# Performance work log

Measured on AMD Instinct MI355X. Metric: run time of the kernel, lower is better.

The kernel has to match this reference:

```python
import jax, jax.numpy as jnp
import numpy as np

DIM = 256
NUM_HEADS = 8
HEAD_DIM = DIM // NUM_HEADS


def rope_sincos(H, W, head_dim, dtype=jnp.float32):
    n = head_dim // 4
    angle = 1.0 / (10000.0 ** jnp.linspace(0.0, 1.0, n))
    angle = jnp.repeat(angle, 2)  # (head_dim//2,)
    ph = jnp.arange(H, dtype=dtype)[:, None] * angle[None, :]  # (H, d/2)
    pw = jnp.arange(W, dtype=dtype)[:, None] * angle[None, :]  # (W, d/2)
    sin_h = jnp.broadcast_to(jnp.sin(ph)[:, None, :], (H, W, 2 * n))
    sin_w = jnp.broadcast_to(jnp.sin(pw)[None, :, :], (H, W, 2 * n))
    cos_h = jnp.broadcast_to(jnp.cos(ph)[:, None, :], (H, W, 2 * n))
    cos_w = jnp.broadcast_to(jnp.cos(pw)[None, :, :], (H, W, 2 * n))
    sin = jnp.concatenate([sin_h, sin_w], -1).reshape(H * W, head_dim)
    cos = jnp.concatenate([cos_h, cos_w], -1).reshape(H * W, head_dim)
    return sin, cos


def rotate_every_two(x):
    x1 = x[..., 0::2]
    x2 = x[..., 1::2]
    return jnp.stack([-x2, x1], axis=-1).reshape(x.shape)


def theta_shift(x, sin, cos):
    return x * cos + rotate_every_two(x) * sin


def conv1x1(x, w, b):
    # x: (B,C,H,W), w: (O,C,1,1)
    return jnp.einsum('bchw,oc->bohw', x, w[:, :, 0, 0]) + b[None, :, None, None]


def depthwise5x5(x, w, b):
    # x: (B,C,H,W), w: (C,1,5,5), groups=C
    y = jax.lax.conv_general_dilated(
        x, w, window_strides=(1, 1), padding=((2, 2), (2, 2)),
        feature_group_count=x.shape[1],
        dimension_numbers=('NCHW', 'OIHW', 'NCHW'))
    return y + b[None, :, None, None]


def setup_inputs() -> dict:
    key = jax.random.key(0)
    ks = jax.random.split(key, 7)
    B, C, H, W = 8, DIM, 64, 64
    x = jax.random.normal(ks[0], (B, C, H, W), dtype=jnp.float32)
    qkvo_w = 0.02 * jax.random.normal(ks[1], (4 * C, C, 1, 1), dtype=jnp.float32)
    qkvo_b = jnp.zeros((4 * C,), dtype=jnp.float32)
    lepe_w = 0.02 * jax.random.normal(ks[2], (C, 1, 5, 5), dtype=jnp.float32)
    lepe_b = jnp.zeros((C,), dtype=jnp.float32)
    proj_w = 0.02 * jax.random.normal(ks[3], (C, C, 1, 1), dtype=jnp.float32)
    proj_b = jnp.zeros((C,), dtype=jnp.float32)
    return {'x': x, 'qkvo_w': qkvo_w, 'qkvo_b': qkvo_b,
            'lepe_w': lepe_w, 'lepe_b': lepe_b,
            'proj_w': proj_w, 'proj_b': proj_b}


def reference(x, qkvo_w, qkvo_b, lepe_w, lepe_b, proj_w, proj_b):
    B, C, H, W = x.shape
    n, d = NUM_HEADS, HEAD_DIM
    L = H * W
    scale = d ** (-0.5)

    sin, cos = rope_sincos(H, W, d, dtype=x.dtype)  # (L, d)

    qkvo = conv1x1(x, qkvo_w, qkvo_b)          # (B, 4C, H, W)
    qkv = qkvo[:, :3 * C]                       # (B, 3C, H, W)
    o = qkvo[:, 3 * C:]                         # (B, C, H, W)
    lepe = depthwise5x5(qkv[:, 2 * C:], lepe_w, lepe_b)  # (B, C, H, W)

    # 'b (m n d) h w -> m b n (h w) d'
    qkv_r = qkv.reshape(B, 3, n, d, H * W).transpose(1, 0, 2, 4, 3)  # (3,B,n,L,d)
    q, k, v = qkv_r[0], qkv_r[1], qkv_r[2]

    q = jax.nn.elu(q) + 1.0
    k = jax.nn.elu(k) + 1.0

    kmean = k.mean(axis=2, keepdims=True)               # (B,n,1,d)
    z = jnp.einsum('bnld,bnmd->bnlm', q, kmean) * scale  # (B,n,L,1)

    q = theta_shift(q, sin, cos)
    k = theta_shift(k, sin, cos)

    c = (scale / L) ** 0.5
    kv = jnp.einsum('bnld,bnle->bnde', k * c, v * c)     # (B,n,d,d)
    vmean = v.mean(axis=2, keepdims=True)                # (B,n,1,d)

    res = jnp.einsum('bnld,bnde->bnle', q, kv) * (1.0 + 1.0 / (z + 1e-6)) - z * vmean
    # 'b n (h w) d -> b (n d) h w'
    res = res.reshape(B, n, H, W, d).transpose(0, 1, 4, 2, 3).reshape(B, C, H, W)
    res = res + lepe
    return conv1x1(res * o, proj_w, proj_b)
```

## Files before the change

### kernel.cpp

```cpp
#include <hip/hip_runtime.h>
#include <math.h>

typedef unsigned short u16;
typedef unsigned int u32;
typedef unsigned long long u64;
typedef __attribute__((ext_vector_type(8))) short short8;
typedef __attribute__((ext_vector_type(4))) float f32x4;
typedef __attribute__((ext_vector_type(16))) float f32x16;

static constexpr float SCALE = 0.17677669529663687f;
static constexpr float C2    = 0.17677669529663687f / 4096.f;

__device__ __forceinline__ float bf2f(u16 u){
  union { u32 i; float f; } v; v.i = ((u32)u) << 16; return v.f;
}
__device__ __forceinline__ u16 f2bf(float f){
  union { float fl; u32 i; } v; v.fl = f;
  u32 r = v.i + 0x7fffu + ((v.i >> 16) & 1u);
  return (u16)(r >> 16);
}
__device__ __forceinline__ float eluP(float x){ return x > 0.f ? x + 1.f : __expf(x); }
__device__ __forceinline__ float rfreq(int j){
  const float t[8] = {1.f, 0.2682695795f, 0.0719685673f, 0.0193069773f,
                      0.0051794747f, 0.0013894955f, 0.0003727594f, 1e-4f};
  return t[j];
}
__device__ __forceinline__ void gload16(const u16* g, u16* l){
  __builtin_amdgcn_global_load_lds(
      (const __attribute__((address_space(1))) u32*)g,
      (__attribute__((address_space(3))) u32*)l, 16, 0, 0);
}

__global__ __launch_bounds__(256) void k_pre(
    const float* __restrict__ x, const float* __restrict__ qw, const float* __restrict__ pw,
    u16* __restrict__ XT, u16* __restrict__ Whi, u16* __restrict__ Wlo,
    u16* __restrict__ Phi, u16* __restrict__ Plo, float* __restrict__ KM0)
{
  if (blockIdx.z < 8){
    __shared__ float t[64][65];
    int l0 = blockIdx.x * 64, c0 = blockIdx.y * 64, b = blockIdx.z;
    const float* xp = x + (((long)b * 256 + c0) << 12) + l0;
    #pragma unroll
    for (int rep = 0; rep < 4; rep++){
      int idx = threadIdx.x + rep * 256;
      int r = idx >> 4, ch = (idx & 15) * 4;
      float4 f = *(const float4*)&xp[((long)r << 12) + ch];
      t[r][ch] = f.x; t[r][ch+1] = f.y; t[r][ch+2] = f.z; t[r][ch+3] = f.w;
    }
    __syncthreads();
    int r2 = threadIdx.x >> 2, c8 = (threadIdx.x & 3) * 16;
    u32 w[8];
    #pragma unroll
    for (int j = 0; j < 8; j++){
      float v0 = t[c8 + 2*j][r2], v1 = t[c8 + 2*j + 1][r2];
      w[j] = (u32)f2bf(v0) | ((u32)f2bf(v1) << 16);
    }
    long ob = (((long)b << 12) << 8) + ((long)(l0 + r2) << 8) + c0 + c8;
    *(uint4*)&XT[ob]     = make_uint4(w[0], w[1], w[2], w[3]);
    *(uint4*)&XT[ob + 8] = make_uint4(w[4], w[5], w[6], w[7]);
  } else {
    int bid = (blockIdx.z - 8) * 256 + blockIdx.y * 64 + blockIdx.x;
    int idx = bid * 256 + threadIdx.x;
    if (idx < 262144){
      float v = qw[idx]; u16 h = f2bf(v);
      Whi[idx] = h; Wlo[idx] = f2bf(v - bf2f(h));
    }
    if (idx < 65536){
      float v = pw[idx]; u16 h = f2bf(v);
      Phi[idx] = h; Plo[idx] = f2bf(v - bf2f(h));
    }
    if (bid == 0){
      #pragma unroll
      for (int i = 0; i < 16; i++) KM0[threadIdx.x + i * 256] = 0.f;
    }
  }
}

__global__ __launch_bounds__(256) void k_gemmA(
    const u16* __restrict__ Whi_, const u16* __restrict__ Wlo_,
    const u16* __restrict__ Bh_,
    const float* __restrict__ bias,
    u16* __restrict__ Q16, u16* __restrict__ K16,
    u16* __restrict__ V16, u16* __restrict__ O16,
    float* __restrict__ KMb, float* __restrict__ VMb)
{
  __shared__ __align__(16) u16 AhS[4096];
  __shared__ __align__(16) u16 AlS[4096];
  __shared__ __align__(16) u16 BhS[4096];
  __shared__ float scs[2][8][64];
  const int tid = threadIdx.x;
  const int nt = blockIdx.x, mt = blockIdx.y, b = blockIdx.z;
  const int m0 = mt * 128, n0 = nt * 128;
  const int wave = tid >> 6, lane = tid & 63;
  const int wm = wave & 1, wn = wave >> 1, qu = lane >> 4, ln = lane & 15;

  #pragma unroll
  for (int r = 0; r < 2; r++){
    int idx = tid + r * 256;
    int jj = idx >> 6, pp = idx & 63;
    float sn, cs; sincosf(rfreq(jj) * (float)pp, &sn, &cs);
    scs[0][jj][pp] = sn; scs[1][jj][pp] = cs;
  }

  const u16* bhp = Bh_ + (((long)b << 12) << 8);

  const int l4 = lane >> 2, c4 = lane & 3;
  const int gch = (c4 ^ (l4 & 3)) * 8;
  const int fch = (qu ^ (ln & 3)) * 8;

  f32x4 acc[4][4];
  #pragma unroll
  for (int im = 0; im < 4; im++)
    #pragma unroll
    for (int in = 0; in < 4; in++)
      #pragma unroll
      for (int r = 0; r < 4; r++) acc[im][in][r] = 0.f;

  for (int kk = 0; kk < 256; kk += 32){
    #pragma unroll
    for (int t = 0; t < 2; t++){
      int rw = wave * 32 + t * 16;
      int ga = (m0 + rw + l4) * 256 + kk + gch;
      long gb = (long)(n0 + rw + l4) * 256 + kk + gch;
      gload16(&Whi_[ga], &AhS[rw * 32]);
      gload16(&Wlo_[ga], &AlS[rw * 32]);
      gload16(&bhp[gb],  &BhS[rw * 32]);
    }
    __syncthreads();
    short8 fbh[4];
    #pragma unroll
    for (int in = 0; in < 4; in++){
      int row = wn * 64 + in * 16 + ln;
      fbh[in] = *(short8*)&BhS[row * 32 + fch];
    }
    #pragma unroll
    for (int im = 0; im < 4; im++){
      int row = wm * 64 + im * 16 + ln;
      short8 fah = *(short8*)&AhS[row * 32 + fch];
      short8 fal = *(short8*)&AlS[row * 32 + fch];
      #pragma unroll
      for (int in = 0; in < 4; in++){
        acc[im][in] = __builtin_amdgcn_mfma_f32_16x16x32_bf16(fah, fbh[in], acc[im][in], 0, 0, 0);
        acc[im][in] = __builtin_amdgcn_mfma_f32_16x16x32_bf16(fal, fbh[in], acc[im][in], 0, 0, 0);
      }
    }
    __syncthreads();
  }

  const int range = m0 >> 8;
  u16* dst = (range == 0) ? Q16 : (range == 1) ? K16 : (range == 2) ? V16 : O16;
  #pragma unroll
  for (int im = 0; im < 4; im++){
    const int mb = m0 + wm * 64 + im * 16 + qu * 4;
    float v[4][4];
    #pragma unroll
    for (int r = 0; r < 4; r++){
      float bia = bias[mb + r];
      #pragma unroll
      for (int in = 0; in < 4; in++){
        float t = acc[im][in][r] + bia;
        v[r][in] = (range < 2) ? eluP(t) : t;
      }
    }
    if (range == 1 || range == 2){
      float* mbuf = (range == 1) ? KMb : VMb;
      #pragma unroll
      for (int r = 0; r < 4; r++){
        float s = v[r][0] + v[r][1] + v[r][2] + v[r][3];
        s += __shfl_xor(s, 1); s += __shfl_xor(s, 2);
        s += __shfl_xor(s, 4); s += __shfl_xor(s, 8);
        if (ln == 0) atomicAdd(&mbuf[b * 256 + ((mb + r) & 255)], s);
      }
    }
    if (range == 1){
      const int p0 = (mb & 31) >> 1;
      #pragma unroll
      for (int half = 0; half < 2; half++){
        int p = p0 + half, j = p & 7;
        #pragma unroll
        for (int in = 0; in < 4; in++){
          int n = n0 + wn * 64 + in * 16 + ln;
          int pos = (p < 8) ? (n >> 6) : (n & 63);
          float sn = scs[0][j][pos], cs = scs[1][j][pos];
          float a = v[2*half][in], bb = v[2*half+1][in];
          v[2*half][in]   = a * cs - bb * sn;
          v[2*half+1][in] = bb * cs + a * sn;
        }
      }
    }
    #pragma unroll
    for (int r = 0; r < 4; r++){
      u16* rowp = dst + (((long)b * 256 + ((mb + r) & 255)) << 12);
      #pragma unroll
      for (int in = 0; in < 4; in++){
        int n = n0 + wn * 64 + in * 16 + ln;
        rowp[n] = f2bf(v[r][in]);
      }
    }
  }
}

__global__ __launch_bounds__(256) void k_mid(
    const u16* __restrict__ K16, const u16* __restrict__ V16,
    const float* __restrict__ lw, const float* __restrict__ lb,
    u16* __restrict__ Tb16, float* __restrict__ KVb)
{
  if (blockIdx.y < 256){
    __shared__ float tile[20][68];
    __shared__ float wl[25];
    int ht = blockIdx.x, ch = blockIdx.y, b = blockIdx.z;
    int h0 = ht * 16;
    const u16* vp = V16 + (((long)b * 256 + ch) << 12);
    if (threadIdx.x < 25) wl[threadIdx.x] = lw[ch * 25 + threadIdx.x];
    for (int idx = threadIdx.x; idx < 20 * 68; idx += 256){
      int r = idx / 68, c = idx % 68;
      int gh = h0 + r - 2, gw = c - 2;
      float v = 0.f;
      if (gh >= 0 && gh < 64 && gw >= 0 && gw < 64) v = bf2f(vp[(gh << 6) + gw]);
      tile[r][c] = v;
    }
    __syncthreads();
    const float bia = lb[ch];
    #pragma unroll
    for (int r2 = 0; r2 < 4; r2++){
      int idx = threadIdx.x + r2 * 256;
      int oh = idx >> 6, ow = idx & 63;
      float s = bia;
      #pragma unroll
      for (int i = 0; i < 5; i++)
        #pragma unroll
        for (int j = 0; j < 5; j++) s += tile[oh + i][ow + j] * wl[i * 5 + j];
      Tb16[(((long)b * 256 + ch) << 12) + ((h0 + oh) << 6) + ow] = f2bf(s);
    }
  } else {
    __shared__ float red[4][1024];
    int kvIdx = (blockIdx.y - 256) * 32 + blockIdx.z * 4 + blockIdx.x;
    int n = kvIdx & 7, b = kvIdx >> 3;
    const int tid = threadIdx.x, wave = tid >> 6, lane = tid & 63;
    const u16* kp = K16 + (((long)(b * 256 + n * 32)) << 12);
    const u16* vp = V16 + (((long)(b * 256 + n * 32)) << 12);
    const int m = lane & 31, kh = lane >> 5;
    const long row = ((long)m << 12);

    f32x16 acc;
    #pragma unroll
    for (int r = 0; r < 16; r++) acc[r] = 0.f;
    #pragma unroll 4
    for (int it = 0; it < 64; it++){
      int l = wave * 1024 + it * 16 + kh * 8;
      short8 a  = *(const short8*)&kp[row + l];
      short8 bf = *(const short8*)&vp[row + l];
      acc = __builtin_amdgcn_mfma_f32_32x32x16_bf16(a, bf, acc, 0, 0, 0);
    }
    #pragma unroll
    for (int reg = 0; reg < 16; reg++){
      int rr = (reg & 3) + 8 * (reg >> 2) + 4 * kh;
      red[wave][rr * 32 + m] = acc[reg];
    }
    __syncthreads();
    #pragma unroll
    for (int i = tid; i < 1024; i += 256){
      float s = red[0][i] + red[1][i] + red[2][i] + red[3][i];
      KVb[(((long)b * 8 + n) << 10) + i] = s * C2;
    }
  }
}

__global__ __launch_bounds__(256) void k_res(
    const u16* __restrict__ Q16, const float* __restrict__ KMb,
    const float* __restrict__ KVb, const float* __restrict__ VMb,
    const u16* __restrict__ O16, const u16* __restrict__ Tb16,
    u16* __restrict__ TT16)
{
  __shared__ __align__(16) float kvs[1024];
  __shared__ float scs[2][8][64];
  __shared__ float kms[32], vms[32];
  __shared__ __align__(16) u64 tts[256 * 9];
  const int b = blockIdx.z, n = blockIdx.y, tid = threadIdx.x;
  #pragma unroll
  for (int r = 0; r < 2; r++){
    int idx = tid + r * 256;
    int jj = idx >> 6, pp = idx & 63;
    float sn, cs; sincosf(rfreq(jj) * (float)pp, &sn, &cs);
    scs[0][jj][pp] = sn; scs[1][jj][pp] = cs;
  }
  {
    const float* kv = KVb + (((long)b * 8 + n) << 10);
    #pragma unroll
    for (int r = 0; r < 4; r++) kvs[tid + r * 256] = kv[tid + r * 256];
    if (tid < 32){
      kms[tid] = KMb[b * 256 + n * 32 + tid] * (1.f / 4096.f);
      vms[tid] = VMb[b * 256 + n * 32 + tid] * (1.f / 4096.f);
    }
  }
  __syncthreads();

  const int l0 = blockIdx.x * 256;
  const int l = l0 + tid;
  const long cbase = ((long)(b * 256 + n * 32)) << 12;

  float q[32];
  #pragma unroll
  for (int d = 0; d < 32; d++) q[d] = bf2f(Q16[cbase + ((long)d << 12) + l]);
  float z = 0.f;
  #pragma unroll
  for (int d = 0; d < 32; d++) z += q[d] * kms[d];
  z *= SCALE;
  #pragma unroll
  for (int p = 0; p < 16; p++){
    int pos = (p < 8) ? (l >> 6) : (l & 63);
    float sn = scs[0][p & 7][pos], cs = scs[1][p & 7][pos];
    float q0 = q[2*p], q1 = q[2*p+1];
    q[2*p]   = q0 * cs - q1 * sn;
    q[2*p+1] = q1 * cs + q0 * sn;
  }

  float acc[32];
  #pragma unroll
  for (int e = 0; e < 32; e++) acc[e] = 0.f;
  #pragma unroll 8
  for (int d = 0; d < 32; d++){
    float qd = q[d];
    #pragma unroll
    for (int ec = 0; ec < 8; ec++){
      float4 kvv = *(float4*)&kvs[d * 32 + ec * 4];
      acc[ec*4+0] += qd * kvv.x;
      acc[ec*4+1] += qd * kvv.y;
      acc[ec*4+2] += qd * kvv.z;
      acc[ec*4+3] += qd * kvv.w;
    }
  }

  const float f = 1.f + 1.f / (z + 1e-6f);
  u32 w[16];
  #pragma unroll
  for (int e = 0; e < 32; e++){
    long off = cbase + ((long)e << 12) + l;
    float val = (acc[e] * f - z * vms[e] + bf2f(Tb16[off])) * bf2f(O16[off]);
    u16 h = f2bf(val);
    if (e & 1) w[e >> 1] |= ((u32)h << 16);
    else       w[e >> 1] = h;
  }
  #pragma unroll
  for (int j = 0; j < 8; j++)
    tts[tid * 9 + j] = (u64)w[2*j] | ((u64)w[2*j+1] << 32);
  __syncthreads();
  #pragma unroll
  for (int it = 0; it < 4; it++){
    int row = (tid >> 2) + 64 * it;
    int cc = tid & 3;
    u64 a  = tts[row * 9 + cc * 2];
    u64 bb = tts[row * 9 + cc * 2 + 1];
    long orow = (((long)b << 12) << 8) + ((long)(l0 + row) << 8) + n * 32 + cc * 8;
    *(uint4*)&TT16[orow] = make_uint4((u32)a, (u32)(a >> 32), (u32)bb, (u32)(bb >> 32));
  }
}

__global__ __launch_bounds__(256) void k_gemmP(
    const u16* __restrict__ Phi_, const u16* __restrict__ Plo_,
    const u16* __restrict__ TT16, const float* __restrict__ bias,
    float* __restrict__ out)
{
  __shared__ __align__(16) u16 AhS[4096];
  __shared__ __align__(16) u16 AlS[4096];
  __shared__ __align__(16) u16 BhS[4096];
  const int tid = threadIdx.x;
  const int nt = blockIdx.x, mt = blockIdx.y, b = blockIdx.z;
  const int m0 = mt * 128, n0 = nt * 128;
  const int wave = tid >> 6, lane = tid & 63;
  const int wm = wave & 1, wn = wave >> 1, qu = lane >> 4, ln = lane & 15;

  const u16* bhp = TT16 + (((long)b << 12) << 8);
  const int l4 = lane >> 2, c4 = lane & 3;
  const int gch = (c4 ^ (l4 & 3)) * 8;
  const int fch = (qu ^ (ln & 3)) * 8;

  f32x4 acc[4][4];
  #pragma unroll
  for (int im = 0; im < 4; im++)
    #pragma unroll
    for (int in = 0; in < 4; in++)
      #pragma unroll
      for (int r = 0; r < 4; r++) acc[im][in][r] = 0.f;

  for (int kk = 0; kk < 256; kk += 32){
    #pragma unroll
    for (int t = 0; t < 2; t++){
      int rw = wave * 32 + t * 16;
      int ga = (m0 + rw + l4) * 256 + kk + gch;
      long gb = (long)(n0 + rw + l4) * 256 + kk + gch;
      gload16(&Phi_[ga], &AhS[rw * 32]);
      gload16(&Plo_[ga], &AlS[rw * 32]);
      gload16(&bhp[gb],  &BhS[rw * 32]);
    }
    __syncthreads();
    short8 fbh[4];
    #pragma unroll
    for (int in = 0; in < 4; in++){
      int row = wn * 64 + in * 16 + ln;
      fbh[in] = *(short8*)&BhS[row * 32 + fch];
    }
    #pragma unroll
    for (int im = 0; im < 4; im++){
      int row = wm * 64 + im * 16 + ln;
      short8 fah = *(short8*)&AhS[row * 32 + fch];
      short8 fal = *(short8*)&AlS[row * 32 + fch];
      #pragma unroll
      for (int in = 0; in < 4; in++){
        acc[im][in] = __builtin_amdgcn_mfma_f32_16x16x32_bf16(fah, fbh[in], acc[im][in], 0, 0, 0);
        acc[im][in] = __builtin_amdgcn_mfma_f32_16x16x32_bf16(fal, fbh[in], acc[im][in], 0, 0, 0);
      }
    }
    __syncthreads();
  }
  #pragma unroll
  for (int im = 0; im < 4; im++){
    int mbase = m0 + wm * 64 + im * 16 + qu * 4;
    #pragma unroll
    for (int r = 0; r < 4; r++){
      int m = mbase + r;
      float bia = bias[m];
      float* row = out + (((long)b * 256 + m) << 12);
      #pragma unroll
      for (int in = 0; in < 4; in++){
        int n = n0 + wn * 64 + in * 16 + ln;
        row[n] = acc[im][in][r] + bia;
      }
    }
  }
}

extern "C" void kernel_launch(void* const* d_in, const int* in_sizes, int n_in,
                              void* d_out, int out_size, void* d_ws, size_t ws_size,
                              hipStream_t stream)
{
  const float* x  = (const float*)d_in[0];
  const float* qw = (const float*)d_in[1];
  const float* qb = (const float*)d_in[2];
  const float* lw = (const float*)d_in[3];
  const float* lb = (const float*)d_in[4];
  const float* pw = (const float*)d_in[5];
  const float* pb = (const float*)d_in[6];

  u16* W    = (u16*)d_ws;
  u16* Q16  = W;
  u16* K16  = Q16 + 8388608;
  u16* V16  = K16 + 8388608;
  u16* O16  = V16 + 8388608;
  u16* Tb16 = O16 + 8388608;
  u16* XT   = Tb16 + 8388608;
  u16* Whi  = XT + 8388608;
  u16* Wlo  = Whi + 262144;
  u16* Phi  = Wlo + 262144;
  u16* Plo  = Phi + 65536;
  float* KMb = (float*)(Plo + 65536);
  float* VMb = KMb + 2048;
  float* KVb = VMb + 2048;
  size_t total_bytes = (6ull*8388608 + 2*262144 + 2*65536) * 2 + (2048+2048+65536) * 4;
  if (ws_size < total_bytes) return;

  u16* TT16 = XT;

  k_pre<<<dim3(64, 4, 12), 256, 0, stream>>>(x, qw, pw, XT, Whi, Wlo, Phi, Plo, KMb);
  k_gemmA<<<dim3(32, 8, 8), 256, 0, stream>>>(Whi, Wlo, XT, qb,
                                              Q16, K16, V16, O16, KMb, VMb);
  k_mid<<<dim3(4, 258, 8), 256, 0, stream>>>(K16, V16, lw, lb, Tb16, KVb);
  k_res<<<dim3(16, 8, 8), 256, 0, stream>>>(Q16, KMb, KVb, VMb, O16, Tb16, TT16);
  k_gemmP<<<dim3(32, 2, 8), 256, 0, stream>>>(Phi, Plo, TT16, pb, (float*)d_out);
}
```

Baseline: 232.5 us.

## Double-buffer LDS tiles in projection GEMMs and adjust swizzle pattern

Both the QKVO and output-projection GEMM kernels now use two LDS buffers, issuing the next K-slice's global-to-LDS loads before computing on the current one, with one barrier per step instead of two. The XOR swizzle now keys on row>>1 rather than row, to change the LDS bank-conflict pattern. The sin/cos table is computed only by K-range blocks, overlapped with the first tile load. LDS use doubles, which may lower occupancy, and whether gload16 is async determines how much real overlap the prefetch gets.

```diff
diff --git a/kernel.cpp b/kernel.cpp
--- a/kernel.cpp
+++ b/kernel.cpp
@@ -84,70 +84,83 @@
     u16* __restrict__ V16, u16* __restrict__ O16,
     float* __restrict__ KMb, float* __restrict__ VMb)
 {
-  __shared__ __align__(16) u16 AhS[4096];
-  __shared__ __align__(16) u16 AlS[4096];
-  __shared__ __align__(16) u16 BhS[4096];
+  __shared__ __align__(16) u16 AhS[2][4096];
+  __shared__ __align__(16) u16 AlS[2][4096];
+  __shared__ __align__(16) u16 BhS[2][4096];
   __shared__ float scs[2][8][64];
   const int tid = threadIdx.x;
   const int nt = blockIdx.x, mt = blockIdx.y, b = blockIdx.z;
   const int m0 = mt * 128, n0 = nt * 128;
   const int wave = tid >> 6, lane = tid & 63;
   const int wm = wave & 1, wn = wave >> 1, qu = lane >> 4, ln = lane & 15;
-
-  #pragma unroll
-  for (int r = 0; r < 2; r++){
-    int idx = tid + r * 256;
-    int jj = idx >> 6, pp = idx & 63;
-    float sn, cs; sincosf(rfreq(jj) * (float)pp, &sn, &cs);
-    scs[0][jj][pp] = sn; scs[1][jj][pp] = cs;
-  }
+  const int range = m0 >> 8;
 
   const u16* bhp = Bh_ + (((long)b << 12) << 8);
 
   const int l4 = lane >> 2, c4 = lane & 3;
-  const int gch = (c4 ^ (l4 & 3)) * 8;
-  const int fch = (qu ^ (ln & 3)) * 8;
-
-  f32x4 acc[4][4];
-  #pragma unroll
-  for (int im = 0; im < 4; im++)
-    #pragma unroll
-    for (int in = 0; in < 4; in++)
-      #pragma unroll
-      for (int r = 0; r < 4; r++) acc[im][in][r] = 0.f;
-
-  for (int kk = 0; kk < 256; kk += 32){
+  const int gch = (c4 ^ ((l4 >> 1) & 3)) * 8;
+  const int fch = (qu ^ ((ln >> 1) & 3)) * 8;
+
+  auto stage = [&](int buf, int kk){
     #pragma unroll
     for (int t = 0; t < 2; t++){
       int rw = wave * 32 + t * 16;
       int ga = (m0 + rw + l4) * 256 + kk + gch;
       long gb = (long)(n0 + rw + l4) * 256 + kk + gch;
-      gload16(&Whi_[ga], &AhS[rw * 32]);
-      gload16(&Wlo_[ga], &AlS[rw * 32]);
-      gload16(&bhp[gb],  &BhS[rw * 32]);
-    }
-    __syncthreads();
+      gload16(&Whi_[ga], &AhS[buf][rw * 32]);
+      gload16(&Wlo_[ga], &AlS[buf][rw * 32]);
+      gload16(&bhp[gb],  &BhS[buf][rw * 32]);
+    }
+  };
+
+  f32x4 acc[4][4];
+  #pragma unroll
+  for (int im = 0; im < 4; im++)
+    #pragma unroll
+    for (int in = 0; in < 4; in++)
+      #pragma unroll
+      for (int r = 0; r < 4; r++) acc[im][in][r] = 0.f;
+
+  stage(0, 0);
+  if (range == 1){
+    #pragma unroll
+    for (int r = 0; r < 2; r++){
+      int idx = tid + r * 256;
+      int jj = idx >> 6, pp = idx & 63;
+      float sn, cs; sincosf(rfreq(jj) * (float)pp, &sn, &cs);
+      scs[0][jj][pp] = sn; scs[1][jj][pp] = cs;
+    }
+  }
+  __syncthreads();
+
+  int cur = 0;
+  #pragma unroll
+  for (int ks = 0; ks < 8; ks++){
+    if (ks < 7) stage(cur ^ 1, (ks + 1) * 32);
+    const u16* Ah = AhS[cur];
+    const u16* Al = AlS[cur];
+    const u16* Bc = BhS[cur];
     short8 fbh[4];
     #pragma unroll
     for (int in = 0; in < 4; in++){
       int row = wn * 64 + in * 16 + ln;
-      fbh[in] = *(short8*)&BhS[row * 32 + fch];
+      fbh[in] = *(const short8*)&Bc[row * 32 + fch];
     }
     #pragma unroll
     for (int im = 0; im < 4; im++){
       int row = wm * 64 + im * 16 + ln;
-      short8 fah = *(short8*)&AhS[row * 32 + fch];
-      short8 fal = *(short8*)&AlS[row * 32 + fch];
+      short8 fah = *(const short8*)&Ah[row * 32 + fch];
+      short8 fal = *(const short8*)&Al[row * 32 + fch];
       #pragma unroll
       for (int in = 0; in < 4; in++){
         acc[im][in] = __builtin_amdgcn_mfma_f32_16x16x32_bf16(fah, fbh[in], acc[im][in], 0, 0, 0);
         acc[im][in] = __builtin_amdgcn_mfma_f32_16x16x32_bf16(fal, fbh[in], acc[im][in], 0, 0, 0);
       }
     }
-    __syncthreads();
-  }
-
-  const int range = m0 >> 8;
+    if (ks < 7) __syncthreads();
+    cur ^= 1;
+  }
+
   u16* dst = (range == 0) ? Q16 : (range == 1) ? K16 : (range == 2) ? V16 : O16;
   #pragma unroll
   for (int im = 0; im < 4; im++){
@@ -361,9 +374,9 @@
     const u16* __restrict__ TT16, const float* __restrict__ bias,
     float* __restrict__ out)
 {
-  __shared__ __align__(16) u16 AhS[4096];
-  __shared__ __align__(16) u16 AlS[4096];
-  __shared__ __align__(16) u16 BhS[4096];
+  __shared__ __align__(16) u16 AhS[2][4096];
+  __shared__ __align__(16) u16 AlS[2][4096];
+  __shared__ __align__(16) u16 BhS[2][4096];
   const int tid = threadIdx.x;
   const int nt = blockIdx.x, mt = blockIdx.y, b = blockIdx.z;
   const int m0 = mt * 128, n0 = nt * 128;
@@ -372,47 +385,60 @@
 
   const u16* bhp = TT16 + (((long)b << 12) << 8);
   const int l4 = lane >> 2, c4 = lane & 3;
-  const int gch = (c4 ^ (l4 & 3)) * 8;
-  const int fch = (qu ^ (ln & 3)) * 8;
-
-  f32x4 acc[4][4];
-  #pragma unroll
-  for (int im = 0; im < 4; im++)
-    #pragma unroll
-    for (int in = 0; in < 4; in++)
-      #pragma unroll
-      for (int r = 0; r < 4; r++) acc[im][in][r] = 0.f;
-
-  for (int kk = 0; kk < 256; kk += 32){
+  const int gch = (c4 ^ ((l4 >> 1) & 3)) * 8;
+  const int fch = (qu ^ ((ln >> 1) & 3)) * 8;
+
+  auto stage = [&](int buf, int kk){
     #pragma unroll
     for (int t = 0; t < 2; t++){
       int rw = wave * 32 + t * 16;
       int ga = (m0 + rw + l4) * 256 + kk + gch;
       long gb = (long)(n0 + rw + l4) * 256 + kk + gch;
-      gload16(&Phi_[ga], &AhS[rw * 32]);
-      gload16(&Plo_[ga], &AlS[rw * 32]);
-      gload16(&bhp[gb],  &BhS[rw * 32]);
-    }
-    __syncthreads();
+      gload16(&Phi_[ga], &AhS[buf][rw * 32]);
+      gload16(&Plo_[ga], &AlS[buf][rw * 32]);
+      gload16(&bhp[gb],  &BhS[buf][rw * 32]);
+    }
+  };
+
+  f32x4 acc[4][4];
+  #pragma unroll
+  for (int im = 0; im < 4; im++)
+    #pragma unroll
+    for (int in = 0; in < 4; in++)
+      #pragma unroll
+      for (int r = 0; r < 4; r++) acc[im][in][r] = 0.f;
+
+  stage(0, 0);
+  __syncthreads();
+
+  int cur = 0;
+  #pragma unroll
+  for (int ks = 0; ks < 8; ks++){
+    if (ks < 7) stage(cur ^ 1, (ks + 1) * 32);
+    const u16* Ah = AhS[cur];
+    const u16* Al = AlS[cur];
+    const u16* Bc = BhS[cur];
     short8 fbh[4];
     #pragma unroll
     for (int in = 0; in < 4; in++){
       int row = wn * 64 + in * 16 + ln;
-      fbh[in] = *(short8*)&BhS[row * 32 + fch];
+      fbh[in] = *(const short8*)&Bc[row * 32 + fch];
     }
     #pragma unroll
     for (int im = 0; im < 4; im++){
       int row = wm * 64 + im * 16 + ln;
-      short8 fah = *(short8*)&AhS[row * 32 + fch];
-      short8 fal = *(short8*)&AlS[row * 32 + fch];
+      short8 fah = *(const short8*)&Ah[row * 32 + fch];
+      short8 fal = *(const short8*)&Al[row * 32 + fch];
       #pragma unroll
       for (int in = 0; in < 4; in++){
         acc[im][in] = __builtin_amdgcn_mfma_f32_16x16x32_bf16(fah, fbh[in], acc[im][in], 0, 0, 0);
         acc[im][in] = __builtin_amdgcn_mfma_f32_16x16x32_bf16(fal, fbh[in], acc[im][in], 0, 0, 0);
       }
     }
-    __syncthreads();
-  }
+    if (ks < 7) __syncthreads();
+    cur ^= 1;
+  }
+
   #pragma unroll
   for (int im = 0; im < 4; im++){
     int mbase = m0 + wm * 64 + im * 16 + qu * 4;
```

Result: no change. 231.8 us (-0.3%).

## Load GEMM MFMA fragments directly from global memory instead of LDS staging

Applied to the files above, without the earlier changes.

Both projection GEMMs stop staging A/B tiles through shared memory with global_load_lds and barriers. Each wave now loads its MFMA fragments straight from global memory into registers, with the K loop fully unrolled. The sincos table in k_gemmA is now built only for the K range, which avoids wasted transcendental work in the other blocks. The aim is to remove LDS traffic and synchronisation, at the cost of redundant global/L2 reads across waves, since data is no longer shared within the block, and higher register pressure.

```diff
diff --git a/kernel.cpp b/kernel.cpp
--- a/kernel.cpp
+++ b/kernel.cpp
@@ -24,11 +24,6 @@
   const float t[8] = {1.f, 0.2682695795f, 0.0719685673f, 0.0193069773f,
                       0.0051794747f, 0.0013894955f, 0.0003727594f, 1e-4f};
   return t[j];
-}
-__device__ __forceinline__ void gload16(const u16* g, u16* l){
-  __builtin_amdgcn_global_load_lds(
-      (const __attribute__((address_space(1))) u32*)g,
-      (__attribute__((address_space(3))) u32*)l, 16, 0, 0);
 }
 
 __global__ __launch_bounds__(256) void k_pre(
@@ -84,29 +79,38 @@
     u16* __restrict__ V16, u16* __restrict__ O16,
     float* __restrict__ KMb, float* __restrict__ VMb)
 {
-  __shared__ __align__(16) u16 AhS[4096];
-  __shared__ __align__(16) u16 AlS[4096];
-  __shared__ __align__(16) u16 BhS[4096];
   __shared__ float scs[2][8][64];
   const int tid = threadIdx.x;
   const int nt = blockIdx.x, mt = blockIdx.y, b = blockIdx.z;
   const int m0 = mt * 128, n0 = nt * 128;
   const int wave = tid >> 6, lane = tid & 63;
   const int wm = wave & 1, wn = wave >> 1, qu = lane >> 4, ln = lane & 15;
-
-  #pragma unroll
-  for (int r = 0; r < 2; r++){
-    int idx = tid + r * 256;
-    int jj = idx >> 6, pp = idx & 63;
-    float sn, cs; sincosf(rfreq(jj) * (float)pp, &sn, &cs);
-    scs[0][jj][pp] = sn; scs[1][jj][pp] = cs;
+  const int range = m0 >> 8;
+
+  if (range == 1){
+    #pragma unroll
+    for (int r = 0; r < 2; r++){
+      int idx = tid + r * 256;
+      int jj = idx >> 6, pp = idx & 63;
+      float sn, cs; sincosf(rfreq(jj) * (float)pp, &sn, &cs);
+      scs[0][jj][pp] = sn; scs[1][jj][pp] = cs;
+    }
+    __syncthreads();
   }
 
   const u16* bhp = Bh_ + (((long)b << 12) << 8);
-
-  const int l4 = lane >> 2, c4 = lane & 3;
-  const int gch = (c4 ^ (l4 & 3)) * 8;
-  const int fch = (qu ^ (ln & 3)) * 8;
+  const u16* ap_h[4]; const u16* ap_l[4]; const u16* bp[4];
+  #pragma unroll
+  for (int im = 0; im < 4; im++){
+    int mrow = m0 + wm * 64 + im * 16 + ln;
+    ap_h[im] = Whi_ + mrow * 256 + qu * 8;
+    ap_l[im] = Wlo_ + mrow * 256 + qu * 8;
+  }
+  #pragma unroll
+  for (int in = 0; in < 4; in++){
+    long nrow = (long)(n0 + wn * 64 + in * 16 + ln);
+    bp[in] = bhp + (nrow << 8) + qu * 8;
+  }
 
   f32x4 acc[4][4];
   #pragma unroll
@@ -116,38 +120,27 @@
       #pragma unroll
       for (int r = 0; r < 4; r++) acc[im][in][r] = 0.f;
 
-  for (int kk = 0; kk < 256; kk += 32){
-    #pragma unroll
-    for (int t = 0; t < 2; t++){
-      int rw = wave * 32 + t * 16;
-      int ga = (m0 + rw + l4) * 256 + kk + gch;
-      long gb = (long)(n0 + rw + l4) * 256 + kk + gch;
-      gload16(&Whi_[ga], &AhS[rw * 32]);
-      gload16(&Wlo_[ga], &AlS[rw * 32]);
-      gload16(&bhp[gb],  &BhS[rw * 32]);
-    }
-    __syncthreads();
-    short8 fbh[4];
-    #pragma unroll
-    for (int in = 0; in < 4; in++){
-      int row = wn * 64 + in * 16 + ln;
-      fbh[in] = *(short8*)&BhS[row * 32 + fch];
-    }
+  #pragma unroll
+  for (int ks = 0; ks < 8; ks++){
+    const int kk = ks * 32;
+    short8 fb[4], fh[4], fl[4];
+    #pragma unroll
+    for (int in = 0; in < 4; in++) fb[in] = *(const short8*)&bp[in][kk];
     #pragma unroll
     for (int im = 0; im < 4; im++){
-      int row = wm * 64 + im * 16 + ln;
-      short8 fah = *(short8*)&AhS[row * 32 + fch];
-      short8 fal = *(short8*)&AlS[row * 32 + fch];
+      fh[im] = *(const short8*)&ap_h[im][kk];
+      fl[im] = *(const short8*)&ap_l[im][kk];
+    }
+    #pragma unroll
+    for (int im = 0; im < 4; im++){
       #pragma unroll
       for (int in = 0; in < 4; in++){
-        acc[im][in] = __builtin_amdgcn_mfma_f32_16x16x32_bf16(fah, fbh[in], acc[im][in], 0, 0, 0);
-        acc[im][in] = __builtin_amdgcn_mfma_f32_16x16x32_bf16(fal, fbh[in], acc[im][in], 0, 0, 0);
-      }
-    }
-    __syncthreads();
-  }
-
-  const int range = m0 >> 8;
+        acc[im][in] = __builtin_amdgcn_mfma_f32_16x16x32_bf16(fh[im], fb[in], acc[im][in], 0, 0, 0);
+        acc[im][in] = __builtin_amdgcn_mfma_f32_16x16x32_bf16(fl[im], fb[in], acc[im][in], 0, 0, 0);
+      }
+    }
+  }
+
   u16* dst = (range == 0) ? Q16 : (range == 1) ? K16 : (range == 2) ? V16 : O16;
   #pragma unroll
   for (int im = 0; im < 4; im++){
@@ -361,9 +354,6 @@
     const u16* __restrict__ TT16, const float* __restrict__ bias,
     float* __restrict__ out)
 {
-  __shared__ __align__(16) u16 AhS[4096];
-  __shared__ __align__(16) u16 AlS[4096];
-  __shared__ __align__(16) u16 BhS[4096];
   const int tid = threadIdx.x;
   const int nt = blockIdx.x, mt = blockIdx.y, b = blockIdx.z;
   const int m0 = mt * 128, n0 = nt * 128;
@@ -371,9 +361,18 @@
   const int wm = wave & 1, wn = wave >> 1, qu = lane >> 4, ln = lane & 15;
 
   const u16* bhp = TT16 + (((long)b << 12) << 8);
-  const int l4 = lane >> 2, c4 = lane & 3;
-  const int gch = (c4 ^ (l4 & 3)) * 8;
-  const int fch = (qu ^ (ln & 3)) * 8;
+  const u16* ap_h[4]; const u16* ap_l[4]; const u16* bp[4];
+  #pragma unroll
+  for (int im = 0; im < 4; im++){
+    int mrow = m0 + wm * 64 + im * 16 + ln;
+    ap_h[im] = Phi_ + mrow * 256 + qu * 8;
+    ap_l[im] = Plo_ + mrow * 256 + qu * 8;
+  }
+  #pragma unroll
+  for (int in = 0; in < 4; in++){
+    long nrow = (long)(n0 + wn * 64 + in * 16 + ln);
+    bp[in] = bhp + (nrow << 8) + qu * 8;
+  }
 
   f32x4 acc[4][4];
   #pragma unroll
@@ -383,36 +382,27 @@
       #pragma unroll
       for (int r = 0; r < 4; r++) acc[im][in][r] = 0.f;
 
-  for (int kk = 0; kk < 256; kk += 32){
-    #pragma unroll
-    for (int t = 0; t < 2; t++){
-      int rw = wave * 32 + t * 16;
-      int ga = (m0 + rw + l4) * 256 + kk + gch;
-      long gb = (long)(n0 + rw + l4) * 256 + kk + gch;
-      gload16(&Phi_[ga], &AhS[rw * 32]);
-      gload16(&Plo_[ga], &AlS[rw * 32]);
-      gload16(&bhp[gb],  &BhS[rw * 32]);
-    }
-    __syncthreads();
-    short8 fbh[4];
-    #pragma unroll
-    for (int in = 0; in < 4; in++){
-      int row = wn * 64 + in * 16 + ln;
-      fbh[in] = *(short8*)&BhS[row * 32 + fch];
-    }
+  #pragma unroll
+  for (int ks = 0; ks < 8; ks++){
+    const int kk = ks * 32;
+    short8 fb[4], fh[4], fl[4];
+    #pragma unroll
+    for (int in = 0; in < 4; in++) fb[in] = *(const short8*)&bp[in][kk];
     #pragma unroll
     for (int im = 0; im < 4; im++){
-      int row = wm * 64 + im * 16 + ln;
-      short8 fah = *(short8*)&AhS[row * 32 + fch];
-      short8 fal = *(short8*)&AlS[row * 32 + fch];
+      fh[im] = *(const short8*)&ap_h[im][kk];
+      fl[im] = *(const short8*)&ap_l[im][kk];
+    }
+    #pragma unroll
+    for (int im = 0; im < 4; im++){
       #pragma unroll
       for (int in = 0; in < 4; in++){
-        acc[im][in] = __builtin_amdgcn_mfma_f32_16x16x32_bf16(fah, fbh[in], acc[im][in], 0, 0, 0);
-        acc[im][in] = __builtin_amdgcn_mfma_f32_16x16x32_bf16(fal, fbh[in], acc[im][in], 0, 0, 0);
-      }
-    }
-    __syncthreads();
-  }
+        acc[im][in] = __builtin_amdgcn_mfma_f32_16x16x32_bf16(fh[im], fb[in], acc[im][in], 0, 0, 0);
+        acc[im][in] = __builtin_amdgcn_mfma_f32_16x16x32_bf16(fl[im], fb[in], acc[im][in], 0, 0, 0);
+      }
+    }
+  }
+
   #pragma unroll
   for (int im = 0; im < 4; im++){
     int mbase = m0 + wm * 64 + im * 16 + qu * 4;
```

Result: slower. 299.1 us (+28.7%).
